# Kernel optimization log

Measured on AMD Instinct MI355X. Metric: run time of the kernel, lower is better.

The kernel has to match this reference:

```python
import jax, jax.numpy as jnp
import numpy as np

B, IN, N_NEURONS, DEG = 16384, 256, 64, 7  # batch, input_dim, output_dim (neurons), max_degree
D = IN * (DEG + 1)  # cumulative Chebyshev basis width per sample


def setup_inputs() -> dict:
    key = jax.random.key(0)
    k1, k2, _ = jax.random.split(key, 3)
    x = jax.random.normal(k1, (B, IN), dtype=jnp.float32)
    # per-neuron least-squares coefficients [(deg+1)*input_dim] -> stored as [N, D]
    coeffs = jax.random.normal(k2, (N_NEURONS, D), dtype=jnp.float32) * 0.05
    # horizontal_weight per neuron (nn.Parameter initialized to ones(1))
    hweights = jnp.ones((N_NEURONS,), dtype=jnp.float32)
    return {"x": x, "coeffs": coeffs, "hweights": hweights}


def _cheb_basis(t, deg):
    """Chebyshev T_0..T_deg via recurrence. t: [B, IN] in [-1,1] -> [B, IN, deg+1]."""
    polys = [jnp.ones_like(t), t]
    for _ in range(2, deg + 1):
        polys.append(2.0 * t * polys[-1] - polys[-2])
    return jnp.stack(polys[: deg + 1], axis=-1)


def reference(x, coeffs, hweights):
    # KANNeuron.forward: tanh squash, then cumulative Chebyshev transform
    t = jnp.tanh(x)  # [B, IN]
    # torch code builds, per input dim, stack of T_0..T_deg then cats over dims:
    # layout is dim-major -> reshape of [B, IN, DEG+1] matches exactly
    T = _cheb_basis(t, DEG).reshape(x.shape[0], D)  # [B, D]
    # per-neuron: hweight_n * (T @ c_n); layer: stack over neurons, sum(dim=0)
    Y = T @ (coeffs * hweights[:, None]).T  # [B, N]
    return Y.sum(axis=1, keepdims=True)  # [B, 1] (source sums stacked neuron outputs)
```

## Files before the change

kernel.cpp:

```cpp
#include <hip/hip_runtime.h>


constexpr int B_SAMPLES = 16384;
constexpr int IN_DIM    = 256;
constexpr int N_NEURONS = 64;
constexpr int DEGP1     = 8;
constexpr int D_FEAT    = IN_DIM * DEGP1;
constexpr int D4        = D_FEAT / 4;

__device__ __forceinline__ float fast_tanh(float v) {
    float e = __expf(2.0f * v);
    return 1.0f - 2.0f * __builtin_amdgcn_rcpf(e + 1.0f);
}

__global__ __launch_bounds__(256) void kan_reduce_w(const float* __restrict__ coeffs,
                                                    const float* __restrict__ hw,
                                                    float* __restrict__ w) {
    const int tid   = threadIdx.x;
    const int d4l   = tid & 15;
    const int chunk = tid >> 4;
    const int d4    = blockIdx.x * 16 + d4l;

    const float4* c4 = reinterpret_cast<const float4*>(coeffs);
    float4 acc = {0.f, 0.f, 0.f, 0.f};
#pragma unroll
    for (int j = 0; j < 4; ++j) {
        const int n = chunk * 4 + j;
        const float h  = hw[n];
        const float4 c = c4[(size_t)n * D4 + d4];
        acc.x = fmaf(c.x, h, acc.x);
        acc.y = fmaf(c.y, h, acc.y);
        acc.z = fmaf(c.z, h, acc.z);
        acc.w = fmaf(c.w, h, acc.w);
    }

    __shared__ float4 part[16][16];
    part[chunk][d4l] = acc;
    __syncthreads();
#pragma unroll
    for (int s = 8; s > 0; s >>= 1) {
        if (chunk < s) {
            float4 a = part[chunk][d4l], b = part[chunk + s][d4l];
            a.x += b.x; a.y += b.y; a.z += b.z; a.w += b.w;
            part[chunk][d4l] = a;
        }
        __syncthreads();
    }
    if (chunk == 0)
        reinterpret_cast<float4*>(w)[d4] = part[0][d4l];
}

constexpr int SPB = 16;

__global__ __launch_bounds__(256) void kan_fwd(const float* __restrict__ x,
                                               const float* __restrict__ w,
                                               float* __restrict__ out) {
    const int tid  = threadIdx.x;
    const int lane = tid & 63;
    const int wv   = tid >> 6;
    const int b0   = blockIdx.x * SPB;

    const float4* w4 = reinterpret_cast<const float4*>(w) + (size_t)lane * 8;
    float4 W[4][2];
#pragma unroll
    for (int j = 0; j < 4; ++j) { W[j][0] = w4[j * 2]; W[j][1] = w4[j * 2 + 1]; }

#pragma unroll
    for (int s = wv; s < SPB; s += 4) {
        const int b = b0 + s;
        float4 xv = reinterpret_cast<const float4*>(x + (size_t)b * IN_DIM)[lane];
        float xs[4] = {xv.x, xv.y, xv.z, xv.w};
        float acc = 0.f;
#pragma unroll
        for (int j = 0; j < 4; ++j) {
            const float t  = fast_tanh(xs[j]);
            const float t2 = 2.f * t;
            const float4 wlo = W[j][0], whi = W[j][1];
            float Tm2 = 1.f, Tm1 = t, T;
            float a = fmaf(wlo.y, t, wlo.x);
            T = t2 * Tm1 - Tm2; a = fmaf(wlo.z, T, a); Tm2 = Tm1; Tm1 = T;
            T = t2 * Tm1 - Tm2; a = fmaf(wlo.w, T, a); Tm2 = Tm1; Tm1 = T;
            T = t2 * Tm1 - Tm2; a = fmaf(whi.x, T, a); Tm2 = Tm1; Tm1 = T;
            T = t2 * Tm1 - Tm2; a = fmaf(whi.y, T, a); Tm2 = Tm1; Tm1 = T;
            T = t2 * Tm1 - Tm2; a = fmaf(whi.z, T, a); Tm2 = Tm1; Tm1 = T;
            T = t2 * Tm1 - Tm2; a = fmaf(whi.w, T, a);
            acc += a;
        }
#pragma unroll
        for (int off = 32; off > 0; off >>= 1)
            acc += __shfl_down(acc, off, 64);
        if (lane == 0) out[b] = acc;
    }
}

extern "C" void kernel_launch(void* const* d_in, const int* in_sizes, int n_in,
                              void* d_out, int out_size, void* d_ws, size_t ws_size,
                              hipStream_t stream) {
    const float* x      = (const float*)d_in[0];
    const float* coeffs = (const float*)d_in[1];
    const float* hw     = (const float*)d_in[2];
    float* out = (float*)d_out;
    float* w   = (float*)d_ws;

    kan_reduce_w<<<D4 / 16, 256, 0, stream>>>(coeffs, hw, w);
    kan_fwd<<<B_SAMPLES / SPB, 256, 0, stream>>>(x, w, out);
}
```

Before: 16.84 us.

## Fuse weight reduction into forward kernel with per-block recomputation

Merges the coefficient-by-hweight reduction and the Chebyshev forward pass into one 1024-thread kernel. Each block redundantly reduces all 64 neuron coefficient rows into shared memory, then evaluates 64 samples. This removes one kernel launch and the workspace round trip. In exchange, every block rereads the full coefficient matrix, which adds large redundant cache traffic.

```diff
diff --git a/kernel.cpp b/kernel.cpp
--- a/kernel.cpp
+++ b/kernel.cpp
@@ -7,25 +7,37 @@
 constexpr int DEGP1     = 8;
 constexpr int D_FEAT    = IN_DIM * DEGP1;
 constexpr int D4        = D_FEAT / 4;
+constexpr int TPB       = 1024;
+constexpr int SPB       = 64;
+constexpr int GRID      = B_SAMPLES / SPB;
 
 __device__ __forceinline__ float fast_tanh(float v) {
     float e = __expf(2.0f * v);
     return 1.0f - 2.0f * __builtin_amdgcn_rcpf(e + 1.0f);
 }
 
-__global__ __launch_bounds__(256) void kan_reduce_w(const float* __restrict__ coeffs,
-                                                    const float* __restrict__ hw,
-                                                    float* __restrict__ w) {
-    const int tid   = threadIdx.x;
-    const int d4l   = tid & 15;
-    const int chunk = tid >> 4;
-    const int d4    = blockIdx.x * 16 + d4l;
+__global__ __launch_bounds__(TPB, 1) void kan_fused(
+        const float* __restrict__ x, const float* __restrict__ coeffs,
+        const float* __restrict__ hw, float* __restrict__ out) {
+    const int tid  = threadIdx.x;
+    const int lane = tid & 63;
+    const int wv   = tid >> 6;
+    const int b0   = blockIdx.x * SPB;
 
+    float4 xv[4];
+#pragma unroll
+    for (int s = 0; s < 4; ++s) {
+        const int b = b0 + wv * 4 + s;
+        xv[s] = reinterpret_cast<const float4*>(x + (size_t)b * IN_DIM)[lane];
+    }
+
+    const int d4   = tid & (D4 - 1);
+    const int half = tid >> 9;
     const float4* c4 = reinterpret_cast<const float4*>(coeffs);
     float4 acc = {0.f, 0.f, 0.f, 0.f};
 #pragma unroll
-    for (int j = 0; j < 4; ++j) {
-        const int n = chunk * 4 + j;
+    for (int j = 0; j < 32; ++j) {
+        const int n = half * 32 + j;
         const float h  = hw[n];
         const float4 c = c4[(size_t)n * D4 + d4];
         acc.x = fmaf(c.x, h, acc.x);
@@ -34,43 +46,27 @@
         acc.w = fmaf(c.w, h, acc.w);
     }
 
-    __shared__ float4 part[16][16];
-    part[chunk][d4l] = acc;
+    __shared__ float4 wpart[2][D4];
+    wpart[half][d4] = acc;
     __syncthreads();
-#pragma unroll
-    for (int s = 8; s > 0; s >>= 1) {
-        if (chunk < s) {
-            float4 a = part[chunk][d4l], b = part[chunk + s][d4l];
-            a.x += b.x; a.y += b.y; a.z += b.z; a.w += b.w;
-            part[chunk][d4l] = a;
-        }
-        __syncthreads();
+    if (tid < D4) {
+        float4 a = wpart[0][tid], b = wpart[1][tid];
+        a.x += b.x; a.y += b.y; a.z += b.z; a.w += b.w;
+        wpart[0][tid] = a;
     }
-    if (chunk == 0)
-        reinterpret_cast<float4*>(w)[d4] = part[0][d4l];
-}
+    __syncthreads();
 
-constexpr int SPB = 16;
-
-__global__ __launch_bounds__(256) void kan_fwd(const float* __restrict__ x,
-                                               const float* __restrict__ w,
-                                               float* __restrict__ out) {
-    const int tid  = threadIdx.x;
-    const int lane = tid & 63;
-    const int wv   = tid >> 6;
-    const int b0   = blockIdx.x * SPB;
-
-    const float4* w4 = reinterpret_cast<const float4*>(w) + (size_t)lane * 8;
     float4 W[4][2];
 #pragma unroll
-    for (int j = 0; j < 4; ++j) { W[j][0] = w4[j * 2]; W[j][1] = w4[j * 2 + 1]; }
+    for (int j = 0; j < 4; ++j) {
+        W[j][0] = wpart[0][lane * 8 + 2 * j];
+        W[j][1] = wpart[0][lane * 8 + 2 * j + 1];
+    }
 
 #pragma unroll
-    for (int s = wv; s < SPB; s += 4) {
-        const int b = b0 + s;
-        float4 xv = reinterpret_cast<const float4*>(x + (size_t)b * IN_DIM)[lane];
-        float xs[4] = {xv.x, xv.y, xv.z, xv.w};
-        float acc = 0.f;
+    for (int s = 0; s < 4; ++s) {
+        const float xs[4] = {xv[s].x, xv[s].y, xv[s].z, xv[s].w};
+        float accb = 0.f;
 #pragma unroll
         for (int j = 0; j < 4; ++j) {
             const float t  = fast_tanh(xs[j]);
@@ -84,12 +80,12 @@
             T = t2 * Tm1 - Tm2; a = fmaf(whi.y, T, a); Tm2 = Tm1; Tm1 = T;
             T = t2 * Tm1 - Tm2; a = fmaf(whi.z, T, a); Tm2 = Tm1; Tm1 = T;
             T = t2 * Tm1 - Tm2; a = fmaf(whi.w, T, a);
-            acc += a;
+            accb += a;
         }
 #pragma unroll
         for (int off = 32; off > 0; off >>= 1)
-            acc += __shfl_down(acc, off, 64);
-        if (lane == 0) out[b] = acc;
+            accb += __shfl_down(accb, off, 64);
+        if (lane == 0) out[b0 + wv * 4 + s] = accb;
     }
 }
 
@@ -100,8 +96,6 @@
     const float* coeffs = (const float*)d_in[1];
     const float* hw     = (const float*)d_in[2];
     float* out = (float*)d_out;
-    float* w   = (float*)d_ws;
 
-    kan_reduce_w<<<D4 / 16, 256, 0, stream>>>(coeffs, hw, w);
-    kan_fwd<<<B_SAMPLES / SPB, 256, 0, stream>>>(x, w, out);
+    kan_fused<<<GRID, TPB, 0, stream>>>(x, coeffs, hw, out);
 }
```

New measurement: 16.95 us. Within noise of the previous version (+0.6%).
